# Kernel optimization log

Hardware: AMD Instinct MI355X
Metric: run time of the kernel (lower is better)

The kernel has to match this reference:

```python
import jax, jax.numpy as jnp
import numpy as np

B, F, BOND, NFREQ, NOUT, INIT_STD = 16384, 256, 16, 4, 1, 0.1


def setup_inputs() -> dict:
    key = jax.random.key(0)
    ks = jax.random.split(key, 10)
    x = jax.random.uniform(ks[0], (B, F), dtype=jnp.float32)
    inp = {"x": x, "frequency_min": jnp.array(1.0, dtype=jnp.float32)}
    d_in = 1 + 2 * NFREQ  # physical leg dim = 9
    n, level = F, 0
    while n > 1:
        n2 = n // 2
        d_out = NOUT if n == 2 else BOND
        # stack all same-level node tensors: [n_pairs, d_left, d_right, d_out]
        inp[f"W{level}"] = jax.random.normal(ks[level + 1], (n2, d_in, d_in, d_out), dtype=jnp.float32) * INIT_STD
        d_in, n, level = d_out, n2, level + 1
    return inp


def reference(x, frequency_min, W0, W1, W2, W3, W4, W5, W6, W7):
    Ws = [W0, W1, W2, W3, W4, W5, W6, W7]
    nfreq = (W0.shape[1] - 1) // 2
    # Fourier feature map: [B, F, 1+2*nfreq]
    xs = (x * frequency_min)[..., None]
    freqs = jnp.arange(1, nfreq + 1, dtype=x.dtype)
    feats = jnp.concatenate(
        [jnp.ones_like(xs), jnp.sin(xs * freqs), jnp.cos(xs * freqs)], axis=-1
    )
    nodes = feats  # [B, n_nodes, d]
    for W in Ws:
        left = nodes[:, 0::2]   # [B, n/2, d]
        right = nodes[:, 1::2]  # [B, n/2, d]
        # batched pairwise bilinear contraction over all nodes of one level
        nodes = jnp.einsum('bni,nijd,bnj->bnd', left, W, right)
    return nodes[:, 0, :]  # [B, NOUT]
```

## Files before the change

### kernel.cpp

```cpp
#include <hip/hip_runtime.h>
#include <math.h>

#define BTOT 16384

typedef __attribute__((ext_vector_type(8))) short s16x8;
typedef __attribute__((ext_vector_type(4))) float f32x4;
typedef __attribute__((ext_vector_type(4))) uint u32x4;
typedef __attribute__((ext_vector_type(2))) float f32x2;
typedef __attribute__((ext_vector_type(2))) uint u32x2;

#define OFF0 0u
#define OFF1 655360u
#define OFF2 1179648u
#define OFF3 1441792u
#define OFF4 1572864u
#define OFF5 1638400u
#define OFF6 1671168u
#define OFF7 1687552u

__device__ __forceinline__ ushort rtn_bf16(float x) {
  uint u = __builtin_bit_cast(uint, x);
  uint r = u + 0x7fffu + ((u >> 16) & 1u);
  return (ushort)(r >> 16);
}

__global__ __launch_bounds__(256) void wprep_kernel(
    const float* __restrict__ W0, const float* __restrict__ W1,
    const float* __restrict__ W2, const float* __restrict__ W3,
    const float* __restrict__ W4, const float* __restrict__ W5,
    const float* __restrict__ W6, const float* __restrict__ W7,
    ushort* __restrict__ U) {
  __shared__ float WL[4096];
  int blk = blockIdx.x;
  const float* Wsrc; ushort* dst; int ktN, din, nsrc; bool dout1 = false;
  if (blk < 128)      { Wsrc = W0 + blk * 1296;         dst = U + OFF0 + (size_t)blk * 5120;         ktN = 5; din = 9;  nsrc = 1296; }
  else if (blk < 192) { Wsrc = W1 + (blk - 128) * 4096; dst = U + OFF1 + (size_t)(blk - 128) * 8192; ktN = 8; din = 16; nsrc = 4096; }
  else if (blk < 224) { Wsrc = W2 + (blk - 192) * 4096; dst = U + OFF2 + (size_t)(blk - 192) * 8192; ktN = 8; din = 16; nsrc = 4096; }
  else if (blk < 240) { Wsrc = W3 + (blk - 224) * 4096; dst = U + OFF3 + (size_t)(blk - 224) * 8192; ktN = 8; din = 16; nsrc = 4096; }
  else if (blk < 248) { Wsrc = W4 + (blk - 240) * 4096; dst = U + OFF4 + (size_t)(blk - 240) * 8192; ktN = 8; din = 16; nsrc = 4096; }
  else if (blk < 252) { Wsrc = W5 + (blk - 248) * 4096; dst = U + OFF5 + (size_t)(blk - 248) * 8192; ktN = 8; din = 16; nsrc = 4096; }
  else if (blk < 254) { Wsrc = W6 + (blk - 252) * 4096; dst = U + OFF6 + (size_t)(blk - 252) * 8192; ktN = 8; din = 16; nsrc = 4096; }
  else                { Wsrc = W7;                      dst = U + OFF7;                              ktN = 8; din = 16; nsrc = 256; dout1 = true; }
  for (int i = threadIdx.x; i < nsrc; i += 256) WL[i] = Wsrc[i];
  __syncthreads();
  int entries = ktN * 512;
  for (int e = threadIdx.x; e < entries; e += 256) {
    int kt = e >> 9, l = (e >> 3) & 63, jv = e & 7;
    int k = kt * 32 + ((l >> 4) << 3) + jv;
    int i = k >> 4, j = k & 15, n = l & 15;
    float w;
    if (dout1) w = (n == 0) ? WL[i * 16 + j] : 0.f;
    else       w = (i < din && j < din) ? WL[(i * din + j) * 16 + n] : 0.f;
    uint u = __builtin_bit_cast(uint, w);
    uint h = u & 0xffff0000u;
    dst[e] = (ushort)(h >> 16);
    dst[entries + e] = rtn_bf16(w - __builtin_bit_cast(float, h));
  }
}

__device__ __forceinline__ f32x4 split3(float li, const f32x2* rf2,
                                        s16x8 wh, s16x8 wl, f32x4 acc) {
  const f32x2 li2 = {li, li};
  u32x4 hv, lv;
#pragma unroll
  for (int jp = 0; jp < 4; ++jp) {
    f32x2 p2 = li2 * rf2[jp];
    u32x2 u2 = __builtin_bit_cast(u32x2, p2);
    u32x2 hb = u2 & 0xffff0000u;
    f32x2 h2 = __builtin_bit_cast(f32x2, hb);
    f32x2 q2 = __builtin_elementwise_fma(li2, rf2[jp], -h2);
    u32x2 uq = __builtin_bit_cast(u32x2, q2);
    hv[jp] = __builtin_amdgcn_perm(u2.y, u2.x, 0x07060302u);
    lv[jp] = __builtin_amdgcn_perm(uq.y, uq.x, 0x07060302u);
  }
  s16x8 ahi = __builtin_bit_cast(s16x8, hv);
  s16x8 alo = __builtin_bit_cast(s16x8, lv);
  acc = __builtin_amdgcn_mfma_f32_16x16x32_bf16(ahi, wh, acc, 0, 0, 0);
  acc = __builtin_amdgcn_mfma_f32_16x16x32_bf16(alo, wh, acc, 0, 0, 0);
  acc = __builtin_amdgcn_mfma_f32_16x16x32_bf16(ahi, wl, acc, 0, 0, 0);
  return acc;
}

template <int KTN, bool L0M>
__device__ __forceinline__ f32x4 mfma_core(const float* Lcol, const float* Rcol,
                                           const int ld, const ushort* __restrict__ Wf,
                                           int lane) {
  const int g = lane >> 4;
  const int j0 = (g & 1) * 8, gh = g >> 1;
  const float* Lg = Lcol + gh * ld;
  float lf[KTN];
#pragma unroll
  for (int i = 0; i < KTN; ++i)
    lf[i] = (L0M && (2 * i + gh > 8)) ? 0.f : Lg[2 * i * ld];
  f32x2 rf2[4];
#pragma unroll
  for (int j = 0; j < 8; ++j) {
    float v = (L0M && (j0 + j >= 9)) ? 0.f : Rcol[(j0 + j) * ld];
    rf2[j >> 1][j & 1] = v;
  }
  f32x4 acc = {0.f, 0.f, 0.f, 0.f};
  const int entries = KTN * 512;
#pragma unroll
  for (int kt = 0; kt < KTN; ++kt) {
    const s16x8 wh = *(const s16x8*)&Wf[(kt * 64 + lane) * 8];
    const s16x8 wl = *(const s16x8*)&Wf[entries + (kt * 64 + lane) * 8];
    acc = split3(lf[kt], rf2, wh, wl, acc);
  }
  return acc;
}

#define LDF 67

__device__ __forceinline__ void feats_col(float xv, float* Fb, int col) {
  float s1 = __sinf(xv), c1 = __cosf(xv);
  Fb[0 * LDF + col] = 1.f; Fb[1 * LDF + col] = s1; Fb[5 * LDF + col] = c1;
  float sk = s1, ck = c1;
#pragma unroll
  for (int k = 2; k <= 4; ++k) {
    float sn = s1 * ck + c1 * sk, cn = c1 * ck - s1 * sk;
    sk = sn; ck = cn;
    Fb[k * LDF + col] = sk; Fb[(4 + k) * LDF + col] = ck;
  }
}

__global__ __launch_bounds__(256, 4) void ttn_front_kernel(
    const float* __restrict__ x, const float* __restrict__ fminp,
    const ushort* __restrict__ U, float* __restrict__ s1out) {
  __shared__ float F0[9 * LDF], F1[9 * LDF];
  __shared__ float A0[16 * LDF], B0[16 * LDF];
  __shared__ float A1[16 * LDF], B1[16 * LDF];
  __shared__ float A2[16 * LDF], B2[16 * LDF];

  const int tid = threadIdx.x;
  const int lane = tid & 63, w = tid >> 6;
  const int m = lane & 15, g = lane >> 4;
  const int bl = w * 16 + m;
  const int b0 = blockIdx.x * 64;
  const int s = blockIdx.y;
  const float fmin = fminp[0];

  const float* xw = x + (size_t)(b0 + w * 16 + (lane & 15)) * 256 + s * 16;
  float* outG = s1out + (size_t)(s * 16) * BTOT + b0;

  auto storeL = [&](f32x4 a, float* Out) {
#pragma unroll
    for (int r = 0; r < 4; ++r) Out[m * LDF + w * 16 + g * 4 + r] = a[r];
  };

  for (int t = 0; t < 8; ++t) {
    if (lane < 32) {
      int side = lane >> 4;
      float xv = xw[2 * t + side] * fmin;
      feats_col(xv, side ? F1 : F0, w * 16 + (lane & 15));
    }
    f32x4 a = mfma_core<5, true>(&F0[bl], &F1[bl], LDF,
                                 U + OFF0 + (size_t)(8 * s + t) * 5120, lane);
    storeL(a, (t & 1) ? B0 : A0);
    if (t & 1) {
      f32x4 c1 = mfma_core<8, false>(&A0[bl], &B0[bl], LDF,
                                     U + OFF1 + (size_t)(4 * s + (t >> 1)) * 8192, lane);
      storeL(c1, ((t >> 1) & 1) ? B1 : A1);
      if ((t & 3) == 3) {
        f32x4 c2 = mfma_core<8, false>(&A1[bl], &B1[bl], LDF,
                                       U + OFF2 + (size_t)(2 * s + (t >> 2)) * 8192, lane);
        storeL(c2, ((t >> 2) & 1) ? B2 : A2);
        if (t == 7) {
          f32x4 c3 = mfma_core<8, false>(&A2[bl], &B2[bl], LDF,
                                         U + OFF3 + (size_t)s * 8192, lane);
#pragma unroll
          for (int r = 0; r < 4; ++r)
            outG[(size_t)m * BTOT + w * 16 + g * 4 + r] = c3[r];
        }
      }
    }
  }
}

__global__ __launch_bounds__(512) void ttn_back_kernel(
    const float* __restrict__ s1, const ushort* __restrict__ U,
    float* __restrict__ out) {
  __shared__ float T[256 * 17];
  __shared__ float P[8][16 * 17];
  const int tid = threadIdx.x;
  const int lane = tid & 63, v = tid >> 6;
  const int m = lane & 15, g = lane >> 4;
  const int b0 = blockIdx.x * 16;

  auto storeC = [&](f32x4 a, float* Buf) {
#pragma unroll
    for (int r = 0; r < 4; ++r) Buf[m * 17 + g * 4 + r] = a[r];
  };

#pragma unroll
  for (int it = 0; it < 2; ++it) {
    int idx = it * 512 + tid;
    int r = idx >> 2, c4 = (idx & 3) * 4;
    float4 vv = *(const float4*)&s1[(size_t)r * BTOT + b0 + c4];
    T[r * 17 + c4 + 0] = vv.x; T[r * 17 + c4 + 1] = vv.y;
    T[r * 17 + c4 + 2] = vv.z; T[r * 17 + c4 + 3] = vv.w;
  }
  __syncthreads();

  {
    f32x4 a = mfma_core<8, false>(&T[(32 * v) * 17 + m], &T[(32 * v + 16) * 17 + m],
                                  17, U + OFF4 + (size_t)v * 8192, lane);
    storeC(a, P[v]);
  }
  __syncthreads();

  if (v < 4) {
    f32x4 a = mfma_core<8, false>(&P[2 * v][m], &P[2 * v + 1][m], 17,
                                  U + OFF5 + (size_t)v * 8192, lane);
    storeC(a, &T[v * 16 * 17]);
  }
  __syncthreads();

  if (v < 2) {
    f32x4 a = mfma_core<8, false>(&T[(2 * v) * 16 * 17 + m],
                                  &T[(2 * v + 1) * 16 * 17 + m], 17,
                                  U + OFF6 + (size_t)v * 8192, lane);
    storeC(a, P[v]);
  }
  __syncthreads();

  if (v == 0) {
    f32x4 a = mfma_core<8, false>(&P[0][m], &P[1][m], 17, U + OFF7, lane);
    if (m == 0) {
#pragma unroll
      for (int r = 0; r < 4; ++r) out[b0 + g * 4 + r] = a[r];
    }
  }
}

extern "C" void kernel_launch(void* const* d_in, const int* in_sizes, int n_in,
                              void* d_out, int out_size, void* d_ws, size_t ws_size,
                              hipStream_t stream) {
  const float* x    = (const float*)d_in[0];
  const float* fmin = (const float*)d_in[1];
  const float* W0   = (const float*)d_in[2];
  const float* W1   = (const float*)d_in[3];
  const float* W2   = (const float*)d_in[4];
  const float* W3   = (const float*)d_in[5];
  const float* W4   = (const float*)d_in[6];
  const float* W5   = (const float*)d_in[7];
  const float* W6   = (const float*)d_in[8];
  const float* W7   = (const float*)d_in[9];
  float* out = (float*)d_out;

  ushort* U = (ushort*)d_ws;
  float* s1 = (float*)((char*)d_ws + (4u << 20));

  wprep_kernel<<<255, 256, 0, stream>>>(W0, W1, W2, W3, W4, W5, W6, W7, U);
  ttn_front_kernel<<<dim3(256, 16), 256, 0, stream>>>(x, fmin, U, s1);
  ttn_back_kernel<<<1024, 512, 0, stream>>>(s1, U, out);
}
```

Measured before the change: 235.4 us.

## Restructure front-level bilinear contraction as left-by-weight MFMA then right scaling

The front kernel's levels 0-3 switch from forming left*right outer products per sample and splitting them into bf16 hi/lo (split3) to a two-step scheme. The left vector is split into hi/lo bf16 as an MFMA A operand, multiplied against per-j weight slices (hi and lo), and the result is scaled by the right feature on VALU and accumulated. Weight prep uses a new per-nt layout with tighter padding for level 0, and shared memory becomes per-wave row-major tiles with vectorized loads. This removes the per-product split arithmetic but adds MFMAs per j-slice and a different precision trade-off.

```diff
diff --git a/kernel.cpp b/kernel.cpp
--- a/kernel.cpp
+++ b/kernel.cpp
@@ -9,14 +9,14 @@
 typedef __attribute__((ext_vector_type(2))) float f32x2;
 typedef __attribute__((ext_vector_type(2))) uint u32x2;
 
-#define OFF0 0u
-#define OFF1 655360u
-#define OFF2 1179648u
-#define OFF3 1441792u
-#define OFF4 1572864u
-#define OFF5 1638400u
-#define OFF6 1671168u
-#define OFF7 1687552u
+#define NOFF0 0u
+#define NOFF1 589824u
+#define NOFF2 1114112u
+#define NOFF3 1376256u
+#define OFF4  1507328u
+#define OFF5  1572864u
+#define OFF6  1605632u
+#define OFF7  1622016u
 
 __device__ __forceinline__ ushort rtn_bf16(float x) {
   uint u = __builtin_bit_cast(uint, x);
@@ -32,29 +32,45 @@
     ushort* __restrict__ U) {
   __shared__ float WL[4096];
   int blk = blockIdx.x;
-  const float* Wsrc; ushort* dst; int ktN, din, nsrc; bool dout1 = false;
-  if (blk < 128)      { Wsrc = W0 + blk * 1296;         dst = U + OFF0 + (size_t)blk * 5120;         ktN = 5; din = 9;  nsrc = 1296; }
-  else if (blk < 192) { Wsrc = W1 + (blk - 128) * 4096; dst = U + OFF1 + (size_t)(blk - 128) * 8192; ktN = 8; din = 16; nsrc = 4096; }
-  else if (blk < 224) { Wsrc = W2 + (blk - 192) * 4096; dst = U + OFF2 + (size_t)(blk - 192) * 8192; ktN = 8; din = 16; nsrc = 4096; }
-  else if (blk < 240) { Wsrc = W3 + (blk - 224) * 4096; dst = U + OFF3 + (size_t)(blk - 224) * 8192; ktN = 8; din = 16; nsrc = 4096; }
-  else if (blk < 248) { Wsrc = W4 + (blk - 240) * 4096; dst = U + OFF4 + (size_t)(blk - 240) * 8192; ktN = 8; din = 16; nsrc = 4096; }
-  else if (blk < 252) { Wsrc = W5 + (blk - 248) * 4096; dst = U + OFF5 + (size_t)(blk - 248) * 8192; ktN = 8; din = 16; nsrc = 4096; }
-  else if (blk < 254) { Wsrc = W6 + (blk - 252) * 4096; dst = U + OFF6 + (size_t)(blk - 252) * 8192; ktN = 8; din = 16; nsrc = 4096; }
-  else                { Wsrc = W7;                      dst = U + OFF7;                              ktN = 8; din = 16; nsrc = 256; dout1 = true; }
-  for (int i = threadIdx.x; i < nsrc; i += 256) WL[i] = Wsrc[i];
-  __syncthreads();
-  int entries = ktN * 512;
-  for (int e = threadIdx.x; e < entries; e += 256) {
-    int kt = e >> 9, l = (e >> 3) & 63, jv = e & 7;
-    int k = kt * 32 + ((l >> 4) << 3) + jv;
-    int i = k >> 4, j = k & 15, n = l & 15;
-    float w;
-    if (dout1) w = (n == 0) ? WL[i * 16 + j] : 0.f;
-    else       w = (i < din && j < din) ? WL[(i * din + j) * 16 + n] : 0.f;
-    uint u = __builtin_bit_cast(uint, w);
-    uint h = u & 0xffff0000u;
-    dst[e] = (ushort)(h >> 16);
-    dst[entries + e] = rtn_bf16(w - __builtin_bit_cast(float, h));
+  if (blk < 240) {
+    const float* Wsrc; ushort* dst; int din, nsrc;
+    if (blk < 128)      { Wsrc = W0 + blk * 1296;         dst = U + NOFF0 + (size_t)blk * 4608;         din = 9;  nsrc = 1296; }
+    else if (blk < 192) { Wsrc = W1 + (blk - 128) * 4096; dst = U + NOFF1 + (size_t)(blk - 128) * 8192; din = 16; nsrc = 4096; }
+    else if (blk < 224) { Wsrc = W2 + (blk - 192) * 4096; dst = U + NOFF2 + (size_t)(blk - 192) * 8192; din = 16; nsrc = 4096; }
+    else                { Wsrc = W3 + (blk - 224) * 4096; dst = U + NOFF3 + (size_t)(blk - 224) * 8192; din = 16; nsrc = 4096; }
+    for (int i = threadIdx.x; i < nsrc; i += 256) WL[i] = Wsrc[i];
+    __syncthreads();
+    int entries = din * 256;
+    for (int e = threadIdx.x; e < entries; e += 256) {
+      int nt = e >> 8, l32 = (e >> 3) & 31, jj = e & 7;
+      int i = ((l32 >> 4) << 3) + jj, d = l32 & 15;
+      float w = (i < din) ? WL[(i * din + nt) * 16 + d] : 0.f;
+      uint u = __builtin_bit_cast(uint, w);
+      uint h = u & 0xffff0000u;
+      dst[e] = (ushort)(h >> 16);
+      dst[entries + e] = rtn_bf16(w - __builtin_bit_cast(float, h));
+    }
+  } else {
+    const float* Wsrc; ushort* dst; int nsrc; bool dout1 = false;
+    if (blk < 248)      { Wsrc = W4 + (blk - 240) * 4096; dst = U + OFF4 + (size_t)(blk - 240) * 8192; nsrc = 4096; }
+    else if (blk < 252) { Wsrc = W5 + (blk - 248) * 4096; dst = U + OFF5 + (size_t)(blk - 248) * 8192; nsrc = 4096; }
+    else if (blk < 254) { Wsrc = W6 + (blk - 252) * 4096; dst = U + OFF6 + (size_t)(blk - 252) * 8192; nsrc = 4096; }
+    else                { Wsrc = W7;                      dst = U + OFF7;                              nsrc = 256; dout1 = true; }
+    for (int i = threadIdx.x; i < nsrc; i += 256) WL[i] = Wsrc[i];
+    __syncthreads();
+    const int entries = 8 * 512;
+    for (int e = threadIdx.x; e < entries; e += 256) {
+      int kt = e >> 9, l = (e >> 3) & 63, jv = e & 7;
+      int k = kt * 32 + ((l >> 4) << 3) + jv;
+      int i = k >> 4, j = k & 15, n = l & 15;
+      float w;
+      if (dout1) w = (n == 0) ? WL[i * 16 + j] : 0.f;
+      else       w = WL[(i * 16 + j) * 16 + n];
+      uint u = __builtin_bit_cast(uint, w);
+      uint h = u & 0xffff0000u;
+      dst[e] = (ushort)(h >> 16);
+      dst[entries + e] = rtn_bf16(w - __builtin_bit_cast(float, h));
+    }
   }
 }
 
@@ -109,64 +125,116 @@
   return acc;
 }
 
-#define LDF 67
-
-__device__ __forceinline__ void feats_col(float xv, float* Fb, int col) {
+#define LDB 20
+
+__device__ __forceinline__ void feats_row(float xv, float* Fr) {
   float s1 = __sinf(xv), c1 = __cosf(xv);
-  Fb[0 * LDF + col] = 1.f; Fb[1 * LDF + col] = s1; Fb[5 * LDF + col] = c1;
-  float sk = s1, ck = c1;
-#pragma unroll
-  for (int k = 2; k <= 4; ++k) {
-    float sn = s1 * ck + c1 * sk, cn = c1 * ck - s1 * sk;
-    sk = sn; ck = cn;
-    Fb[k * LDF + col] = sk; Fb[(4 + k) * LDF + col] = ck;
-  }
+  float s2 = s1 * c1 + c1 * s1, c2 = c1 * c1 - s1 * s1;
+  float s3 = s1 * c2 + c1 * s2, c3 = c1 * c2 - s1 * s2;
+  float s4 = s1 * c3 + c1 * s3, c4 = c1 * c3 - s1 * s3;
+  f32x4 v0 = {1.f, s1, s2, s3};
+  f32x4 v1 = {s4, c1, c2, c3};
+  *(f32x4*)(Fr) = v0;
+  *(f32x4*)(Fr + 4) = v1;
+  Fr[8] = c4;
+}
+
+template <int NT>
+__device__ __forceinline__ f32x4 core2(const float* Lb, const float* Rb,
+                                       const ushort* __restrict__ Wf, int lane) {
+  const int bb = lane & 15, g = lane >> 4;
+  const float* lp = Lb + bb * LDB + (g & 1) * 8;
+  f32x4 v0 = *(const f32x4*)lp;
+  f32x4 v1 = *(const f32x4*)(lp + 4);
+  u32x4 u0 = __builtin_bit_cast(u32x4, v0);
+  u32x4 u1 = __builtin_bit_cast(u32x4, v1);
+  u32x4 hv;
+  if (g < 2) {
+    hv[0] = __builtin_amdgcn_perm(u0.y, u0.x, 0x07060302u);
+    hv[1] = __builtin_amdgcn_perm(u0.w, u0.z, 0x07060302u);
+    hv[2] = __builtin_amdgcn_perm(u1.y, u1.x, 0x07060302u);
+    hv[3] = __builtin_amdgcn_perm(u1.w, u1.z, 0x07060302u);
+  } else {
+    u32x4 h0 = u0 & 0xffff0000u, h1 = u1 & 0xffff0000u;
+    f32x4 q0 = v0 - __builtin_bit_cast(f32x4, h0);
+    f32x4 q1 = v1 - __builtin_bit_cast(f32x4, h1);
+    u32x4 w0 = __builtin_bit_cast(u32x4, q0), w1 = __builtin_bit_cast(u32x4, q1);
+    hv[0] = __builtin_amdgcn_perm(w0.y, w0.x, 0x07060302u);
+    hv[1] = __builtin_amdgcn_perm(w0.w, w0.z, 0x07060302u);
+    hv[2] = __builtin_amdgcn_perm(w1.y, w1.x, 0x07060302u);
+    hv[3] = __builtin_amdgcn_perm(w1.w, w1.z, 0x07060302u);
+  }
+  s16x8 a = __builtin_bit_cast(s16x8, hv);
+  const ushort* whp = Wf + (lane & 31) * 8;
+  const float* rp = Rb + (g * 4) * LDB;
+  f32x4 o = {0.f, 0.f, 0.f, 0.f};
+  const f32x4 zz = {0.f, 0.f, 0.f, 0.f};
+#pragma unroll
+  for (int c = 0; c < (NT + 3) >> 2; ++c) {
+    f32x4 rv0 = *(const f32x4*)(rp + c * 4);
+    f32x4 rv1 = *(const f32x4*)(rp + LDB + c * 4);
+    f32x4 rv2 = *(const f32x4*)(rp + 2 * LDB + c * 4);
+    f32x4 rv3 = *(const f32x4*)(rp + 3 * LDB + c * 4);
+#pragma unroll
+    for (int jj = 0; jj < 4; ++jj) {
+      const int nt = c * 4 + jj;
+      if (nt < NT) {
+        s16x8 wh = *(const s16x8*)(whp + nt * 256);
+        s16x8 wl = *(const s16x8*)(whp + (NT + nt) * 256);
+        f32x4 tt = __builtin_amdgcn_mfma_f32_16x16x32_bf16(a, wh, zz, 0, 0, 0);
+        tt = __builtin_amdgcn_mfma_f32_16x16x32_bf16(a, wl, tt, 0, 0, 0);
+        o[0] += rv0[jj] * tt[0];
+        o[1] += rv1[jj] * tt[1];
+        o[2] += rv2[jj] * tt[2];
+        o[3] += rv3[jj] * tt[3];
+      }
+    }
+  }
+  return o;
 }
 
 __global__ __launch_bounds__(256, 4) void ttn_front_kernel(
     const float* __restrict__ x, const float* __restrict__ fminp,
     const ushort* __restrict__ U, float* __restrict__ s1out) {
-  __shared__ float F0[9 * LDF], F1[9 * LDF];
-  __shared__ float A0[16 * LDF], B0[16 * LDF];
-  __shared__ float A1[16 * LDF], B1[16 * LDF];
-  __shared__ float A2[16 * LDF], B2[16 * LDF];
-
+  __shared__ float S[4][8][16 * LDB];
   const int tid = threadIdx.x;
   const int lane = tid & 63, w = tid >> 6;
   const int m = lane & 15, g = lane >> 4;
-  const int bl = w * 16 + m;
   const int b0 = blockIdx.x * 64;
   const int s = blockIdx.y;
   const float fmin = fminp[0];
 
-  const float* xw = x + (size_t)(b0 + w * 16 + (lane & 15)) * 256 + s * 16;
+  float* F0 = S[w][0]; float* F1 = S[w][1];
+  float* A0 = S[w][2]; float* B0 = S[w][3];
+  float* A1 = S[w][4]; float* B1 = S[w][5];
+  float* A2 = S[w][6]; float* B2 = S[w][7];
+
+  if (lane < 32) {
+    float* Fz = g ? F1 : F0;
+    Fz[m * LDB + 9] = 0.f; Fz[m * LDB + 10] = 0.f; Fz[m * LDB + 11] = 0.f;
+    *(f32x4*)(Fz + m * LDB + 12) = (f32x4){0.f, 0.f, 0.f, 0.f};
+  }
+
+  const float* xrow = x + (size_t)(b0 + w * 16 + m) * 256 + s * 16;
   float* outG = s1out + (size_t)(s * 16) * BTOT + b0;
 
-  auto storeL = [&](f32x4 a, float* Out) {
-#pragma unroll
-    for (int r = 0; r < 4; ++r) Out[m * LDF + w * 16 + g * 4 + r] = a[r];
+  auto storeO = [&](f32x4 a, float* Out) {
+#pragma unroll
+    for (int r = 0; r < 4; ++r) Out[(g * 4 + r) * LDB + m] = a[r];
   };
 
   for (int t = 0; t < 8; ++t) {
-    if (lane < 32) {
-      int side = lane >> 4;
-      float xv = xw[2 * t + side] * fmin;
-      feats_col(xv, side ? F1 : F0, w * 16 + (lane & 15));
-    }
-    f32x4 a = mfma_core<5, true>(&F0[bl], &F1[bl], LDF,
-                                 U + OFF0 + (size_t)(8 * s + t) * 5120, lane);
-    storeL(a, (t & 1) ? B0 : A0);
+    if (lane < 32) feats_row(xrow[2 * t + g] * fmin, (g ? F1 : F0) + m * LDB);
+    f32x4 c0 = core2<9>(F0, F1, U + NOFF0 + (size_t)(8 * s + t) * 4608, lane);
+    storeO(c0, (t & 1) ? B0 : A0);
     if (t & 1) {
-      f32x4 c1 = mfma_core<8, false>(&A0[bl], &B0[bl], LDF,
-                                     U + OFF1 + (size_t)(4 * s + (t >> 1)) * 8192, lane);
-      storeL(c1, ((t >> 1) & 1) ? B1 : A1);
+      f32x4 c1 = core2<16>(A0, B0, U + NOFF1 + (size_t)(4 * s + (t >> 1)) * 8192, lane);
+      storeO(c1, ((t >> 1) & 1) ? B1 : A1);
       if ((t & 3) == 3) {
-        f32x4 c2 = mfma_core<8, false>(&A1[bl], &B1[bl], LDF,
-                                       U + OFF2 + (size_t)(2 * s + (t >> 2)) * 8192, lane);
-        storeL(c2, ((t >> 2) & 1) ? B2 : A2);
+        f32x4 c2 = core2<16>(A1, B1, U + NOFF2 + (size_t)(2 * s + (t >> 2)) * 8192, lane);
+        storeO(c2, ((t >> 2) & 1) ? B2 : A2);
         if (t == 7) {
-          f32x4 c3 = mfma_core<8, false>(&A2[bl], &B2[bl], LDF,
-                                         U + OFF3 + (size_t)s * 8192, lane);
+          f32x4 c3 = core2<16>(A2, B2, U + NOFF3 + (size_t)s * 8192, lane);
 #pragma unroll
           for (int r = 0; r < 4; ++r)
             outG[(size_t)m * BTOT + w * 16 + g * 4 + r] = c3[r];
```

After: 337.5 us. +43.4%, slower.
